# Kernel optimization log

Hardware: AMD Instinct MI355X
Metric: run time of the kernel (lower is better)

The kernel has to match this reference:

```python
import jax, jax.numpy as jnp
import numpy as np

B, N, E, H = 8, 512, 128, 64


def setup_inputs() -> dict:
    key = jax.random.key(0)
    k1, k2, k3 = jax.random.split(key, 3)
    h_freq = jax.random.normal(k1, (B * N, E), dtype=jnp.float32)
    W = jax.random.normal(k2, (2 * E, H), dtype=jnp.float32) * 0.05  # Linear(2E -> H) weight, stored input-major
    b = jnp.zeros((H,), dtype=jnp.float32)
    att = jax.random.normal(k3, (H,), dtype=jnp.float32) * 0.1
    return {"h_freq": h_freq, "W": W, "b": b, "att": att, "batch": B, "n_nodes": N}


def reference(h_freq, W, b, att, batch, n_nodes):
    n = n_nodes
    bsz = h_freq.shape[0] // n
    h = h_freq.reshape(bsz, n, -1)  # [B, N, E]
    # Fused form of cat([hj, hk]) @ W: split W into the hj-half and hk-half.
    W1, W2 = W[: h.shape[-1]], W[h.shape[-1]:]
    pj = h @ W1  # [B, N, H]
    pk = h @ W2  # [B, N, H]
    u = jax.nn.leaky_relu(pj[:, :, None, :] + pk[:, None, :, :] + b, negative_slope=0.2)  # [B, N, N, H]
    e = jnp.einsum("bjkh,h->bjk", u, att)  # [B, N, N]
    alpha = jax.nn.softmax(e, axis=2)
    # dense_to_sparse with learn_sys=True: symmetrize, drop diagonal (eval mode: no dropout)
    dense = (alpha + jnp.swapaxes(alpha, -1, -2)) * 0.5
    mask = ~np.eye(n, dtype=bool)
    src, dst = np.nonzero(mask)  # static, length n*(n-1)
    src = jnp.asarray(src, dtype=jnp.int64)
    dst = jnp.asarray(dst, dtype=jnp.int64)
    single = jnp.stack([src, dst], axis=0)  # [2, M]
    offsets = (jnp.arange(bsz, dtype=jnp.int64) * n)
    edge_index = (single[:, None, :] + offsets[None, :, None]).reshape(2, -1)  # [2, B*M]
    edge_weights = dense[:, src, dst].reshape(-1)  # [B*M]
    return edge_index, edge_weights, alpha
```

## Files before the change

kernel.cpp:

```cpp
#include <hip/hip_runtime.h>
#include <hip/hip_bf16.h>

#define BB 8
#define NN 512
#define EE 128
#define HH 64
#define EP (NN * (NN - 1))
#define ECNT (BB * EP)
#define OFF_EI0 0
#define OFF_EI1 ECNT
#define OFF_EW  (2 * ECNT)
#define OFF_AL  (3 * ECNT)

__global__ void k_proj(const float* __restrict__ h, const float* __restrict__ W,
                       const float* __restrict__ bvec,
                       float* __restrict__ pj, float* __restrict__ pkT) {
    __shared__ float hrow[EE];
    const int i = blockIdx.x;
    const int c = threadIdx.x;
    hrow[c]      = h[i * EE + c];
    hrow[c + 64] = h[i * EE + 64 + c];
    __syncthreads();
    float accj = 0.f, acck = 0.f;
#pragma unroll 8
    for (int e = 0; e < EE; ++e) {
        const float hv = hrow[e];
        accj = fmaf(hv, W[e * HH + c], accj);
        acck = fmaf(hv, W[(EE + e) * HH + c], acck);
    }
    pj[i * HH + c] = accj + bvec[c];
    const int b = i >> 9;
    const int n = i & 511;
    pkT[((size_t)b * HH + c) * NN + n] = acck;
}

__global__ __launch_bounds__(512, 4) void k_attn(
        const float* __restrict__ pj, const float* __restrict__ pkT,
        const float* __restrict__ att, float* __restrict__ alpha) {
    const int bid   = blockIdx.x;
    const int b     = bid >> 6;
    const int jbase = (bid & 63) * 8;
    const int tid   = threadIdx.x;
    const int lane  = tid & 63;
    const int wid   = tid >> 6;

    __shared__ float  pj_s[8][HH];
    __shared__ float4 ap4[HH / 4];
    __shared__ float4 an4[HH / 4];
    __shared__ float  e_s[8][NN];

    pj_s[wid][lane] = pj[((size_t)b * NN + jbase + wid) * HH + lane];
    if (tid < HH / 4) {
        float4 a = reinterpret_cast<const float4*>(att)[tid];
        ap4[tid] = a;
        float4 an; an.x = 0.2f * a.x; an.y = 0.2f * a.y; an.z = 0.2f * a.z; an.w = 0.2f * a.w;
        an4[tid] = an;
    }

    float pkr[HH];
    const float* pkb = pkT + (size_t)b * HH * NN + tid;
#pragma unroll
    for (int hh = 0; hh < HH; ++hh) pkr[hh] = pkb[hh * NN];

    __syncthreads();

    float acc0[8], acc1[8];
#pragma unroll
    for (int j = 0; j < 8; ++j) { acc0[j] = 0.f; acc1[j] = 0.f; }

#pragma unroll
    for (int q = 0; q < HH / 4; ++q) {
        const float4 ap = ap4[q];
        const float4 an = an4[q];
        const float k0 = pkr[4 * q + 0];
        const float k1 = pkr[4 * q + 1];
        const float k2 = pkr[4 * q + 2];
        const float k3 = pkr[4 * q + 3];
#pragma unroll
        for (int j = 0; j < 8; ++j) {
            const float4 pw = reinterpret_cast<const float4*>(&pj_s[j][0])[q];
            float s;
            s = pw.x + k0; acc0[j] = fmaf(s, (s > 0.f) ? ap.x : an.x, acc0[j]);
            s = pw.y + k1; acc1[j] = fmaf(s, (s > 0.f) ? ap.y : an.y, acc1[j]);
            s = pw.z + k2; acc0[j] = fmaf(s, (s > 0.f) ? ap.z : an.z, acc0[j]);
            s = pw.w + k3; acc1[j] = fmaf(s, (s > 0.f) ? ap.w : an.w, acc1[j]);
        }
    }

#pragma unroll
    for (int j = 0; j < 8; ++j) e_s[j][tid] = acc0[j] + acc1[j];
    __syncthreads();

    {
        float v[8];
        float m = -1e30f;
#pragma unroll
        for (int i2 = 0; i2 < 8; ++i2) {
            v[i2] = e_s[wid][lane + 64 * i2];
            m = fmaxf(m, v[i2]);
        }
#pragma unroll
        for (int off = 32; off >= 1; off >>= 1) m = fmaxf(m, __shfl_xor(m, off, 64));
        float s = 0.f;
#pragma unroll
        for (int i2 = 0; i2 < 8; ++i2) { v[i2] = __expf(v[i2] - m); s += v[i2]; }
#pragma unroll
        for (int off = 32; off >= 1; off >>= 1) s += __shfl_xor(s, off, 64);
        const float inv = 1.0f / s;
        float* arow = alpha + ((size_t)b * NN + jbase + wid) * NN;
#pragma unroll
        for (int i2 = 0; i2 < 8; ++i2) arow[lane + 64 * i2] = v[i2] * inv;
    }
}

__global__ void k_edges(const float* __restrict__ alpha, float* __restrict__ out) {
    const int bid   = blockIdx.x;
    const int b     = bid >> 6;
    const int jt    = (bid >> 3) & 7;
    const int kt    = bid & 7;
    const int jbase = jt * 64;
    const int kbase = kt * 64;
    const int tid   = threadIdx.x;
    const int c     = tid & 63;
    const int r0    = tid >> 6;

    __shared__ float at[64][65];

    const float* A = alpha + (size_t)b * NN * NN;

#pragma unroll
    for (int i = 0; i < 16; ++i) {
        const int r = i * 4 + r0;
        at[c][r] = A[(kbase + r) * NN + jbase + c];
    }
    __syncthreads();

    const float fb = (float)(b * NN);
#pragma unroll
    for (int i = 0; i < 16; ++i) {
        const int jj = i * 4 + r0;
        const int j  = jbase + jj;
        const int k  = kbase + c;
        if (k == j) continue;
        const float w = 0.5f * (A[j * NN + k] + at[jj][c]);
        const unsigned t   = (unsigned)k - ((k > j) ? 1u : 0u);
        const unsigned idx = (unsigned)b * EP + (unsigned)j * (NN - 1) + t;
        out[OFF_EI0 + idx] = fb + (float)j;
        out[OFF_EI1 + idx] = fb + (float)k;
        out[OFF_EW  + idx] = w;
    }
}

extern "C" void kernel_launch(void* const* d_in, const int* in_sizes, int n_in,
                              void* d_out, int out_size, void* d_ws, size_t ws_size,
                              hipStream_t stream) {
    const float* h    = (const float*)d_in[0];
    const float* W    = (const float*)d_in[1];
    const float* bvec = (const float*)d_in[2];
    const float* att  = (const float*)d_in[3];
    float* out = (float*)d_out;

    float* pj  = (float*)d_ws;
    float* pkT = pj + (size_t)BB * NN * HH;

    float* alpha = out + OFF_AL;

    k_proj <<<BB * NN, 64, 0, stream>>>(h, W, bvec, pj, pkT);
    k_attn <<<BB * 64, 512, 0, stream>>>(pj, pkT, att, alpha);
    k_edges<<<BB * 64, 256, 0, stream>>>(alpha, out);
}
```

Baseline: 47.26 us.

## Rewrite leaky-ReLU attention as linear plus abs term, precompute linear parts

Uses leaky_relu(s) = 0.6*s + 0.4*|s| so the attention score splits into a linear term, precomputed per node in the projection kernel as cj and dk through a wave reduction, plus an abs-weighted sum. The inner loop becomes add, abs and fma with no compare or select. The projection kernel now computes 8 rows per 256-thread block so each W load is reused across two rows. The attention kernel reads pj and att directly from global memory with uniform addresses instead of staging them in shared memory, dropping one barrier but relying on scalar or cached loads.

```diff
diff --git a/kernel.cpp b/kernel.cpp
--- a/kernel.cpp
+++ b/kernel.cpp
@@ -12,31 +12,64 @@
 #define OFF_EW  (2 * ECNT)
 #define OFF_AL  (3 * ECNT)
 
-__global__ void k_proj(const float* __restrict__ h, const float* __restrict__ W,
-                       const float* __restrict__ bvec,
-                       float* __restrict__ pj, float* __restrict__ pkT) {
-    __shared__ float hrow[EE];
-    const int i = blockIdx.x;
-    const int c = threadIdx.x;
-    hrow[c]      = h[i * EE + c];
-    hrow[c + 64] = h[i * EE + 64 + c];
-    __syncthreads();
-    float accj = 0.f, acck = 0.f;
-#pragma unroll 8
+__global__ __launch_bounds__(256) void k_proj(
+        const float* __restrict__ h, const float* __restrict__ W,
+        const float* __restrict__ bvec, const float* __restrict__ att,
+        float* __restrict__ pj, float* __restrict__ pkT,
+        float* __restrict__ cj, float* __restrict__ dk) {
+    const int row0 = blockIdx.x * 8;
+    const int tid  = threadIdx.x;
+    const int c    = tid & 63;
+    const int w    = __builtin_amdgcn_readfirstlane(tid >> 6);
+
+    const float* hA = h + (size_t)(row0 + w) * EE;
+    const float* hB = h + (size_t)(row0 + w + 4) * EE;
+
+    float aj0 = 0.f, ak0 = 0.f, aj1 = 0.f, ak1 = 0.f;
+#pragma unroll
     for (int e = 0; e < EE; ++e) {
-        const float hv = hrow[e];
-        accj = fmaf(hv, W[e * HH + c], accj);
-        acck = fmaf(hv, W[(EE + e) * HH + c], acck);
-    }
-    pj[i * HH + c] = accj + bvec[c];
-    const int b = i >> 9;
-    const int n = i & 511;
-    pkT[((size_t)b * HH + c) * NN + n] = acck;
+        const float w1 = W[e * HH + c];
+        const float w2 = W[(EE + e) * HH + c];
+        const float h0 = hA[e];
+        const float h1 = hB[e];
+        aj0 = fmaf(h0, w1, aj0);
+        ak0 = fmaf(h0, w2, ak0);
+        aj1 = fmaf(h1, w1, aj1);
+        ak1 = fmaf(h1, w2, ak1);
+    }
+    const float bb = bvec[c];
+    aj0 += bb; aj1 += bb;
+
+    const float a6 = 0.6f * att[c];
+
+    const int iA = row0 + w;
+    const int iB = row0 + w + 4;
+    pj[iA * HH + c] = aj0;
+    pj[iB * HH + c] = aj1;
+    {
+        const int bA = iA >> 9, nA = iA & 511;
+        const int bB = iB >> 9, nB = iB & 511;
+        pkT[((size_t)bA * HH + c) * NN + nA] = ak0;
+        pkT[((size_t)bB * HH + c) * NN + nB] = ak1;
+    }
+    float c0 = a6 * aj0, d0 = a6 * ak0, c1 = a6 * aj1, d1 = a6 * ak1;
+#pragma unroll
+    for (int off = 32; off >= 1; off >>= 1) {
+        c0 += __shfl_xor(c0, off, 64);
+        d0 += __shfl_xor(d0, off, 64);
+        c1 += __shfl_xor(c1, off, 64);
+        d1 += __shfl_xor(d1, off, 64);
+    }
+    if (c == 0) {
+        cj[iA] = c0; dk[iA] = d0;
+        cj[iB] = c1; dk[iB] = d1;
+    }
 }
 
 __global__ __launch_bounds__(512, 4) void k_attn(
         const float* __restrict__ pj, const float* __restrict__ pkT,
-        const float* __restrict__ att, float* __restrict__ alpha) {
+        const float* __restrict__ att, const float* __restrict__ cj,
+        const float* __restrict__ dk, float* __restrict__ alpha) {
     const int bid   = blockIdx.x;
     const int b     = bid >> 6;
     const int jbase = (bid & 63) * 8;
@@ -44,51 +77,48 @@
     const int lane  = tid & 63;
     const int wid   = tid >> 6;
 
-    __shared__ float  pj_s[8][HH];
-    __shared__ float4 ap4[HH / 4];
-    __shared__ float4 an4[HH / 4];
-    __shared__ float  e_s[8][NN];
-
-    pj_s[wid][lane] = pj[((size_t)b * NN + jbase + wid) * HH + lane];
-    if (tid < HH / 4) {
-        float4 a = reinterpret_cast<const float4*>(att)[tid];
-        ap4[tid] = a;
-        float4 an; an.x = 0.2f * a.x; an.y = 0.2f * a.y; an.z = 0.2f * a.z; an.w = 0.2f * a.w;
-        an4[tid] = an;
-    }
+    __shared__ float e_s[8][NN];
 
     float pkr[HH];
     const float* pkb = pkT + (size_t)b * HH * NN + tid;
 #pragma unroll
     for (int hh = 0; hh < HH; ++hh) pkr[hh] = pkb[hh * NN];
-
-    __syncthreads();
-
-    float acc0[8], acc1[8];
-#pragma unroll
-    for (int j = 0; j < 8; ++j) { acc0[j] = 0.f; acc1[j] = 0.f; }
+    const float dkv = dk[b * NN + tid];
+
+    const float* pjb = pj + ((size_t)b * NN + jbase) * HH;
+    const float* cjb = cj + b * NN + jbase;
+
+    float acc[8];
+#pragma unroll
+    for (int j = 0; j < 8; ++j) acc[j] = 0.f;
 
 #pragma unroll
     for (int q = 0; q < HH / 4; ++q) {
-        const float4 ap = ap4[q];
-        const float4 an = an4[q];
+        const float a0 = att[4 * q + 0];
+        const float a1 = att[4 * q + 1];
+        const float a2 = att[4 * q + 2];
+        const float a3 = att[4 * q + 3];
         const float k0 = pkr[4 * q + 0];
         const float k1 = pkr[4 * q + 1];
         const float k2 = pkr[4 * q + 2];
         const float k3 = pkr[4 * q + 3];
 #pragma unroll
         for (int j = 0; j < 8; ++j) {
-            const float4 pw = reinterpret_cast<const float4*>(&pj_s[j][0])[q];
+            const float p0 = pjb[j * HH + 4 * q + 0];
+            const float p1 = pjb[j * HH + 4 * q + 1];
+            const float p2 = pjb[j * HH + 4 * q + 2];
+            const float p3 = pjb[j * HH + 4 * q + 3];
             float s;
-            s = pw.x + k0; acc0[j] = fmaf(s, (s > 0.f) ? ap.x : an.x, acc0[j]);
-            s = pw.y + k1; acc1[j] = fmaf(s, (s > 0.f) ? ap.y : an.y, acc1[j]);
-            s = pw.z + k2; acc0[j] = fmaf(s, (s > 0.f) ? ap.z : an.z, acc0[j]);
-            s = pw.w + k3; acc1[j] = fmaf(s, (s > 0.f) ? ap.w : an.w, acc1[j]);
+            s = p0 + k0; acc[j] = fmaf(a0, fabsf(s), acc[j]);
+            s = p1 + k1; acc[j] = fmaf(a1, fabsf(s), acc[j]);
+            s = p2 + k2; acc[j] = fmaf(a2, fabsf(s), acc[j]);
+            s = p3 + k3; acc[j] = fmaf(a3, fabsf(s), acc[j]);
         }
     }
 
 #pragma unroll
-    for (int j = 0; j < 8; ++j) e_s[j][tid] = acc0[j] + acc1[j];
+    for (int j = 0; j < 8; ++j)
+        e_s[j][tid] = fmaf(0.4f, acc[j], cjb[j] + dkv);
     __syncthreads();
 
     {
@@ -162,10 +192,12 @@
 
     float* pj  = (float*)d_ws;
     float* pkT = pj + (size_t)BB * NN * HH;
+    float* cj  = pkT + (size_t)BB * NN * HH;
+    float* dk  = cj + BB * NN;
 
     float* alpha = out + OFF_AL;
 
-    k_proj <<<BB * NN, 64, 0, stream>>>(h, W, bvec, pj, pkT);
-    k_attn <<<BB * 64, 512, 0, stream>>>(pj, pkT, att, alpha);
+    k_proj <<<BB * NN / 8, 256, 0, stream>>>(h, W, bvec, att, pj, pkT, cj, dk);
+    k_attn <<<BB * 64, 512, 0, stream>>>(pj, pkT, att, cj, dk, alpha);
     k_edges<<<BB * 64, 256, 0, stream>>>(alpha, out);
 }
```

New measurement: 39.97 us. -15.4%, faster.
